# Kernel tuning notes

Measured on AMD Instinct MI355X. Metric: run time of the kernel, lower is better.

Reference implementation:

```python
import jax, jax.numpy as jnp
import numpy as np

B, NV, NQ, D, H = 8, 1024, 512, 1024, 8
HEAD_DIM = D // H


def _linear(x, W, b):
    # torch nn.Linear: x @ W.T + b, W: [out, in]
    return x @ W.T + b


def setup_inputs() -> dict:
    key = jax.random.key(0)
    ks = jax.random.split(key, 10)
    s = 0.02
    f32 = jnp.float32
    return {
        "v": jax.random.normal(ks[0], (B, NV, D), f32),
        "q": jax.random.normal(ks[1], (B, NQ, D), f32),
        "Wg_v4q": jax.random.normal(ks[2], (D, D), f32) * s,
        "bg_v4q": jnp.zeros((D,), f32),
        "Wg_q4v": jax.random.normal(ks[3], (D, D), f32) * s,
        "bg_q4v": jnp.zeros((D,), f32),
        "Wv": jax.random.normal(ks[4], (3 * D, D), f32) * s,
        "bv": jnp.zeros((3 * D,), f32),
        "Wq": jax.random.normal(ks[5], (3 * D, D), f32) * s,
        "bq": jnp.zeros((3 * D,), f32),
        "Wvo": jax.random.normal(ks[6], (D, D), f32) * s,
        "bvo": jnp.zeros((D,), f32),
        "Wqo": jax.random.normal(ks[7], (D, D), f32) * s,
        "bqo": jnp.zeros((D,), f32),
    }


def _mha(qh, kh, vh):
    # qh/kh/vh: [B, N, D] -> head-batched attention, faithful to per-head loop + concat
    b, n, _ = qh.shape
    m = kh.shape[1]
    qh = qh.reshape(b, n, H, HEAD_DIM)
    kh = kh.reshape(b, m, H, HEAD_DIM)
    vh = vh.reshape(b, m, H, HEAD_DIM)
    scores = jnp.einsum("bnhd,bmhd->bhnm", qh, kh) / jnp.sqrt(jnp.float32(HEAD_DIM))
    attn = jax.nn.softmax(scores, axis=-1)
    out = jnp.einsum("bhnm,bmhd->bnhd", attn, vh)
    return out.reshape(b, n, D)


def reference(v, q, Wg_v4q, bg_v4q, Wg_q4v, bg_q4v, Wv, bv, Wq, bq, Wvo, bvo, Wqo, bqo):
    # DyIntraModalityUpdate.forward (drop=0.0)
    v_mean = v.mean(axis=1)
    q_mean = q.mean(axis=1)
    v4q_gate = jax.nn.sigmoid(_linear(jax.nn.relu(v_mean), Wg_v4q, bg_v4q))[:, None, :]
    q4v_gate = jax.nn.sigmoid(_linear(jax.nn.relu(q_mean), Wg_q4v, bg_q4v))[:, None, :]
    v_trans = _linear(jax.nn.relu(v), Wv, bv)
    q_trans = _linear(jax.nn.relu(q), Wq, bq)
    v_k, v_q, v_v = jnp.split(v_trans, 3, axis=2)
    q_k, q_q, q_v = jnp.split(q_trans, 3, axis=2)
    new_vq = (1.0 + q4v_gate) * v_q
    new_vk = (1.0 + q4v_gate) * v_k
    new_qq = (1.0 + v4q_gate) * q_q
    new_qk = (1.0 + v4q_gate) * q_k
    v_update = _mha(new_vq, new_vk, v_v)
    q_update = _mha(new_qq, new_qk, q_v)
    updated_v = _linear(v + v_update, Wvo, bvo)
    updated_q = _linear(q + q_update, Wqo, bqo)
    return (updated_v, updated_q)
```

## Files before the change

kernel.cpp:

```cpp
#include <hip/hip_runtime.h>

typedef unsigned short u16;
typedef unsigned int u32;
typedef __attribute__((ext_vector_type(8))) short short8;
typedef __attribute__((ext_vector_type(4))) float floatx4;

__device__ __forceinline__ float bf2f(u16 x) {
    union { u32 u; float f; } c; c.u = ((u32)x) << 16; return c.f;
}
__device__ __forceinline__ u16 f2bf(float f) {
    union { float f; u32 u; } c; c.f = f;
    return (u16)((c.u + 0x7FFFu + ((c.u >> 16) & 1u)) >> 16);
}
__device__ __forceinline__ u32 pack_bf16(float lo, float hi) {
    return ((u32)f2bf(lo)) | (((u32)f2bf(hi)) << 16);
}

#define GLD_LDS(g, l) __builtin_amdgcn_global_load_lds( \
    (const __attribute__((address_space(1))) u32*)(g),  \
    (__attribute__((address_space(3))) u32*)(l), 16, 0, 0)


__global__ void cvt_kernel(const float* __restrict__ src, u16* __restrict__ dst,
                           int n8, int do_relu) {
    int i = blockIdx.x * 256 + threadIdx.x;
    if (i >= n8) return;
    float4 a = ((const float4*)src)[2 * i];
    float4 b = ((const float4*)src)[2 * i + 1];
    float v[8] = {a.x, a.y, a.z, a.w, b.x, b.y, b.z, b.w};
    short8 o;
#pragma unroll
    for (int j = 0; j < 8; j++) {
        float x = v[j];
        if (do_relu) x = fmaxf(x, 0.f);
        o[j] = (short)f2bf(x);
    }
    ((short8*)dst)[i] = o;
}


__global__ void mean_kernel(const float* __restrict__ x, float* __restrict__ out,
                            int N, int chunk) {
    int idx = blockIdx.x * 256 + threadIdx.x;
    int b = idx >> 10, d = idx & 1023;
    int nlo = blockIdx.y * chunk;
    const float* p = x + (size_t)b * N * 1024 + (size_t)nlo * 1024 + d;
    float s = 0.f;
    for (int n = 0; n < chunk; n++) s += p[(size_t)n * 1024];
    atomicAdd(out + idx, s * (1.0f / (float)N));
}

__global__ __launch_bounds__(256) void gate_kernel(const float* __restrict__ mean,
                                                   const float* __restrict__ Wg,
                                                   const float* __restrict__ bg,
                                                   float* __restrict__ gout) {
    int gw = blockIdx.x * 4 + (threadIdx.x >> 6);
    int lane = threadIdx.x & 63;
    int b = gw >> 10, n = gw & 1023;
    const float* wr = Wg + (size_t)n * 1024;
    const float* mr = mean + b * 1024;
    float acc = 0.f;
    for (int k = lane; k < 1024; k += 64)
        acc += fmaxf(mr[k], 0.f) * wr[k];
#pragma unroll
    for (int m = 1; m < 64; m <<= 1) acc += __shfl_xor(acc, m, 64);
    if (lane == 0) {
        float xg = acc + bg[n];
        gout[gw] = 1.f + 1.f / (1.f + __expf(-xg));
    }
}


__global__ __launch_bounds__(256) void gemm_bt_kernel(
    const u16* __restrict__ A, const u16* __restrict__ W,
    const float* __restrict__ bias, const float* __restrict__ gate,
    u16* __restrict__ Ch, float* __restrict__ Cf,
    int M, int N, int K, int seq, int gateN)
{
    __shared__ u16 As[2][128 * 32];
    __shared__ u16 Bs[2][128 * 32];

    const int tid = threadIdx.x;
    const int wave = tid >> 6, lane = tid & 63, quad = lane >> 4, l15 = lane & 15;

    const u32 gx = gridDim.x;
    const u32 flat = blockIdx.y * gx + blockIdx.x;
    const u32 per = (gx * gridDim.y) >> 3;
    const u32 swz = (flat & 7) * per + (flat >> 3);
    const int m0 = (int)(swz / gx) * 128, n0 = (int)(swz % gx) * 128;

    const int wm = (wave >> 1) * 64, wn = (wave & 1) * 64;

    floatx4 acc[4][4] = {};

    const int e0 = (wave * 1024 + lane * 16) >> 1;
    const int sr0 = e0 >> 5, sc0 = e0 & 31;
    const int e1 = e0 + 2048;
    const int sr1 = e1 >> 5, sc1 = e1 & 31;
    const size_t aoff0 = (size_t)(m0 + sr0) * K + sc0;
    const size_t aoff1 = (size_t)(m0 + sr1) * K + sc1;
    const size_t boff0 = (size_t)(n0 + sr0) * K + sc0;
    const size_t boff1 = (size_t)(n0 + sr1) * K + sc1;

    GLD_LDS(A + aoff0, As[0] + wave * 512);
    GLD_LDS(A + aoff1, As[0] + 2048 + wave * 512);
    GLD_LDS(W + boff0, Bs[0] + wave * 512);
    GLD_LDS(W + boff1, Bs[0] + 2048 + wave * 512);
    __syncthreads();

    int cur = 0;
    for (int k0 = 0; k0 < K; k0 += 32) {
        const int nxt = cur ^ 1;
        if (k0 + 32 < K) {
            GLD_LDS(A + aoff0 + k0 + 32, As[nxt] + wave * 512);
            GLD_LDS(A + aoff1 + k0 + 32, As[nxt] + 2048 + wave * 512);
            GLD_LDS(W + boff0 + k0 + 32, Bs[nxt] + wave * 512);
            GLD_LDS(W + boff1 + k0 + 32, Bs[nxt] + 2048 + wave * 512);
        }

        short8 af[4], bfr[4];
#pragma unroll
        for (int i = 0; i < 4; i++) {
            af[i]  = *(const short8*)(As[cur] + (wm + i * 16 + l15) * 32 + quad * 8);
            bfr[i] = *(const short8*)(Bs[cur] + (wn + i * 16 + l15) * 32 + quad * 8);
        }
#pragma unroll
        for (int mi = 0; mi < 4; mi++)
#pragma unroll
            for (int ni = 0; ni < 4; ni++)
                acc[mi][ni] = __builtin_amdgcn_mfma_f32_16x16x32_bf16(af[mi], bfr[ni], acc[mi][ni], 0, 0, 0);
        __syncthreads();
        cur = nxt;
    }

    const int b = m0 / seq;
#pragma unroll
    for (int ni = 0; ni < 4; ni++) {
        const int ncol = n0 + wn + ni * 16 + l15;
        const float bsv = bias[ncol];
        float g = 1.f;
        if (gate != nullptr && ncol < gateN) g = gate[b * 1024 + (ncol & 1023)];
#pragma unroll
        for (int mi = 0; mi < 4; mi++) {
            const int row = m0 + wm + mi * 16 + quad * 4;
#pragma unroll
            for (int r = 0; r < 4; r++) {
                float val = (acc[mi][ni][r] + bsv) * g;
                size_t idx = (size_t)(row + r) * N + ncol;
                if (Cf) Cf[idx] = val; else Ch[idx] = f2bf(val);
            }
        }
    }
}


__global__ __launch_bounds__(512, 2) void attn_kernel(
    const u16* __restrict__ T, const float* __restrict__ X,
    u16* __restrict__ U, int N)
{
    __shared__ __align__(16) u16 Ks[2][64 * 128];
    __shared__ __align__(16) u16 Vs[2][128 * 64];

    const int tid = threadIdx.x;
    const int wave = tid >> 6, lane = tid & 63, quad = (lane >> 4) & 3, l15 = lane & 15;

    const int f = blockIdx.y * gridDim.x + blockIdx.x;
    const int i3 = f >> 3;
    const int qb = i3 % gridDim.x;
    const int bh = (f & 7) * 8 + i3 / gridDim.x;
    const int b = bh >> 3, h = bh & 7;

    const size_t base = (size_t)b * N * 3072;
    const int kcol = h * 128, qcol = 1024 + h * 128, vcol = 2048 + h * 128;

    short8 qf[4];
    const int qrow0 = qb * 128 + wave * 16;
#pragma unroll
    for (int c = 0; c < 4; c++)
        qf[c] = *(const short8*)(T + base + (size_t)(qrow0 + l15) * 3072
                                   + qcol + c * 32 + quad * 8);

    floatx4 o[8] = {};
    float mrow = -1e30f, lrow = 0.f;
    const float scale = 0.08838834764831845f;

    int kst_kv[2], kst_d[2];
#pragma unroll
    for (int r = 0; r < 2; r++) {
        int ob = r * 8192 + wave * 1024 + lane * 16;
        int kv = ob >> 8;
        kst_kv[r] = kv;
        kst_d[r] = ((((ob >> 4) & 15) ^ (kv & 15)) << 3);
    }
    const int vkv = (tid & 31) * 2;
    const int vd8 = tid >> 5;

    short8 v0, v1;
#pragma unroll
    for (int r = 0; r < 2; r++)
        GLD_LDS(T + base + (size_t)kst_kv[r] * 3072 + kcol + kst_d[r],
                Ks[0] + r * 4096 + wave * 512);
    {
        const u16* vp = T + base + (size_t)vkv * 3072 + vcol + vd8 * 8;
        v0 = *(const short8*)vp;
        v1 = *(const short8*)(vp + 3072);
    }
#pragma unroll
    for (int j = 0; j < 8; j++) {
        u32 wv = ((u32)(u16)v0[j]) | (((u32)(u16)v1[j]) << 16);
        *(u32*)((char*)Vs[0] + (size_t)(vd8 * 8 + j) * 128
                + ((((vkv >> 3) ^ j)) << 4) + ((vkv * 2) & 15)) = wv;
    }
    __syncthreads();

    int cur = 0;
    for (int kt = 0; kt < N; kt += 64) {
        const int nxt = cur ^ 1;
        const bool more = (kt + 64) < N;

        if (more) {
#pragma unroll
            for (int r = 0; r < 2; r++)
                GLD_LDS(T + base + (size_t)(kt + 64 + kst_kv[r]) * 3072 + kcol + kst_d[r],
                        Ks[nxt] + r * 4096 + wave * 512);
            const u16* vp = T + base + (size_t)(kt + 64 + vkv) * 3072 + vcol + vd8 * 8;
            v0 = *(const short8*)vp;
            v1 = *(const short8*)(vp + 3072);
        }

        float p[4][4];
        __builtin_amdgcn_s_setprio(1);
#pragma unroll
        for (int ni = 0; ni < 4; ni++) {
            short8 kf[4];
#pragma unroll
            for (int c = 0; c < 4; c++)
                kf[c] = *(const short8*)(Ks[cur] + (ni * 16 + l15) * 128
                                            + (((c * 4 + quad) ^ l15) << 3));
            floatx4 s = {0.f, 0.f, 0.f, 0.f};
#pragma unroll
            for (int c = 0; c < 4; c++)
                s = __builtin_amdgcn_mfma_f32_16x16x32_bf16(kf[c], qf[c], s, 0, 0, 0);
#pragma unroll
            for (int r = 0; r < 4; r++) p[ni][r] = s[r] * scale;
        }
        __builtin_amdgcn_s_setprio(0);

        {
            float tm = p[0][0];
#pragma unroll
            for (int ni = 0; ni < 4; ni++)
#pragma unroll
                for (int r = 0; r < 4; r++) tm = fmaxf(tm, p[ni][r]);
            tm = fmaxf(tm, __shfl_xor(tm, 16, 64));
            tm = fmaxf(tm, __shfl_xor(tm, 32, 64));
            const bool need = __any(tm > mrow + 8.f);
            if (need) {
                float mnew = fmaxf(mrow, tm);
                float alpha = __expf(mrow - mnew);
                mrow = mnew;
                float ps = 0.f;
#pragma unroll
                for (int ni = 0; ni < 4; ni++)
#pragma unroll
                    for (int r = 0; r < 4; r++) {
                        float pe = __expf(p[ni][r] - mnew);
                        p[ni][r] = pe;
                        ps += pe;
                    }
                ps += __shfl_xor(ps, 16, 64);
                ps += __shfl_xor(ps, 32, 64);
                lrow = lrow * alpha + ps;
#pragma unroll
                for (int r = 0; r < 4; r++) {
                    float ab = __shfl(alpha, quad * 4 + r, 64);
#pragma unroll
                    for (int nt = 0; nt < 8; nt++) o[nt][r] *= ab;
                }
            } else {
                float ps = 0.f;
#pragma unroll
                for (int ni = 0; ni < 4; ni++)
#pragma unroll
                    for (int r = 0; r < 4; r++) {
                        float pe = __expf(p[ni][r] - mrow);
                        p[ni][r] = pe;
                        ps += pe;
                    }
                ps += __shfl_xor(ps, 16, 64);
                ps += __shfl_xor(ps, 32, 64);
                lrow += ps;
            }
        }

        u32* pw = (u32*)((char*)Vs[nxt] + wave * 2048);
        const int xs = (l15 & 7) << 2;
#pragma unroll
        for (int ni = 0; ni < 4; ni++)
#pragma unroll
            for (int s2 = 0; s2 < 2; s2++)
                pw[l15 * 32 + ((ni * 8 + quad * 2 + s2) ^ xs)]
                    = pack_bf16(p[ni][2 * s2], p[ni][2 * s2 + 1]);
        short8 pf[2];
#pragma unroll
        for (int kc = 0; kc < 2; kc++)
            pf[kc] = *(const short8*)(pw + l15 * 32 + ((kc * 16 + quad * 4) ^ xs));

        __builtin_amdgcn_s_setprio(1);
#pragma unroll
        for (int nt = 0; nt < 8; nt++) {
#pragma unroll
            for (int kc = 0; kc < 2; kc++) {
                short8 vf = *(const short8*)(Vs[cur] + (nt * 16 + l15) * 64
                                + (((kc * 4 + quad) ^ (l15 & 7)) << 3));
                o[nt] = __builtin_amdgcn_mfma_f32_16x16x32_bf16(pf[kc], vf, o[nt], 0, 0, 0);
            }
        }
        __builtin_amdgcn_s_setprio(0);

        if (more) {
#pragma unroll
            for (int j = 0; j < 8; j++) {
                u32 wv = ((u32)(u16)v0[j]) | (((u32)(u16)v1[j]) << 16);
                *(u32*)((char*)Vs[nxt] + (size_t)(vd8 * 8 + j) * 128
                        + ((((vkv >> 3) ^ j)) << 4) + ((vkv * 2) & 15)) = wv;
            }
        }
        __syncthreads();
        cur = nxt;
    }

    const size_t ub = (size_t)b * N * 1024;
#pragma unroll
    for (int r = 0; r < 4; r++) {
        float lb = __shfl(lrow, quad * 4 + r, 64);
        float inv = 1.f / lb;
        const size_t row = qb * 128 + wave * 16 + quad * 4 + r;
#pragma unroll
        for (int nt = 0; nt < 8; nt++) {
            const size_t idx = ub + row * 1024 + h * 128 + nt * 16 + l15;
            U[idx] = f2bf(X[idx] + o[nt][r] * inv);
        }
    }
}


extern "C" void kernel_launch(void* const* d_in, const int* in_sizes, int n_in,
                              void* d_out, int out_size, void* d_ws, size_t ws_size,
                              hipStream_t stream) {
    (void)in_sizes; (void)n_in; (void)out_size; (void)ws_size;
    const float* v   = (const float*)d_in[0];
    const float* q   = (const float*)d_in[1];
    const float* Wg_v4q = (const float*)d_in[2];
    const float* bg_v4q = (const float*)d_in[3];
    const float* Wg_q4v = (const float*)d_in[4];
    const float* bg_q4v = (const float*)d_in[5];
    const float* Wv  = (const float*)d_in[6];
    const float* bv  = (const float*)d_in[7];
    const float* Wq  = (const float*)d_in[8];
    const float* bq  = (const float*)d_in[9];
    const float* Wvo = (const float*)d_in[10];
    const float* bvo = (const float*)d_in[11];
    const float* Wqo = (const float*)d_in[12];
    const float* bqo = (const float*)d_in[13];
    float* out = (float*)d_out;

    char* w = (char*)d_ws;
    float* vmean = (float*)(w + 0);
    float* qmean = (float*)(w + 32768);
    float* gv4q  = (float*)(w + 65536);
    float* gq4v  = (float*)(w + 98304);
    u16* cWt  = (u16*)(w + (1 << 20));
    u16* cWo  = (u16*)(w + (1 << 20) + 6291456);
    u16* aReg = (u16*)(w + (16 << 20));
    u16* tReg = (u16*)(w + (32 << 20));

    hipMemsetAsync(vmean, 0, 65536, stream);
    mean_kernel<<<dim3(32, 8), 256, 0, stream>>>(v, vmean, 1024, 128);
    mean_kernel<<<dim3(32, 8), 256, 0, stream>>>(q, qmean, 512, 64);
    gate_kernel<<<2048, 256, 0, stream>>>(vmean, Wg_v4q, bg_v4q, gv4q);
    gate_kernel<<<2048, 256, 0, stream>>>(qmean, Wg_q4v, bg_q4v, gq4v);

    u16* crq  = aReg;
    u16* qt   = tReg;
    u16* qres = aReg;
    cvt_kernel<<<2048, 256, 0, stream>>>(q, crq, 524288, 1);
    cvt_kernel<<<1536, 256, 0, stream>>>(Wq, cWt, 393216, 0);
    cvt_kernel<<<512, 256, 0, stream>>>(Wqo, cWo, 131072, 0);
    gemm_bt_kernel<<<dim3(24, 32), 256, 0, stream>>>(crq, cWt, bq, gv4q, qt, nullptr,
                                                     4096, 3072, 1024, 512, 2048);
    attn_kernel<<<dim3(4, 64), 512, 0, stream>>>(qt, q, qres, 512);
    gemm_bt_kernel<<<dim3(8, 32), 256, 0, stream>>>(qres, cWo, bqo, nullptr, nullptr,
                                                    out + 8388608, 4096, 1024, 1024, 512, 0);

    u16* crv  = aReg;
    u16* vt   = tReg;
    u16* vres = aReg;
    cvt_kernel<<<4096, 256, 0, stream>>>(v, crv, 1048576, 1);
    cvt_kernel<<<1536, 256, 0, stream>>>(Wv, cWt, 393216, 0);
    cvt_kernel<<<512, 256, 0, stream>>>(Wvo, cWo, 131072, 0);
    gemm_bt_kernel<<<dim3(24, 64), 256, 0, stream>>>(crv, cWt, bv, gq4v, vt, nullptr,
                                                     8192, 3072, 1024, 1024, 2048);
    attn_kernel<<<dim3(8, 64), 512, 0, stream>>>(vt, v, vres, 1024);
    gemm_bt_kernel<<<dim3(8, 64), 256, 0, stream>>>(vres, cWo, bvo, nullptr, nullptr,
                                                    out, 8192, 1024, 1024, 1024, 0);
}
```

Measured before the change: 538.4 us.

## Fuse mean reduction with relu-bf16 conversion and batch gate and weight-convert launches

Mean computation for v and q now happens in the same pass that converts the activations to relu'd bf16. Partial sums go to a per-chunk buffer instead of atomics, which also removes the memset. The two gate GEMVs are merged into one launch, and the paired weight conversions are merged as well. This cuts a full extra read of v and q plus several launches. The cost is column-strided 2-byte stores in the fused kernel and a larger workspace so both converted activation buffers can exist at once.

```diff
diff --git a/kernel.cpp b/kernel.cpp
--- a/kernel.cpp
+++ b/kernel.cpp
@@ -21,53 +21,79 @@
     (__attribute__((address_space(3))) u32*)(l), 16, 0, 0)
 
 
-__global__ void cvt_kernel(const float* __restrict__ src, u16* __restrict__ dst,
-                           int n8, int do_relu) {
-    int i = blockIdx.x * 256 + threadIdx.x;
-    if (i >= n8) return;
-    float4 a = ((const float4*)src)[2 * i];
-    float4 b = ((const float4*)src)[2 * i + 1];
-    float v[8] = {a.x, a.y, a.z, a.w, b.x, b.y, b.z, b.w};
-    short8 o;
-#pragma unroll
-    for (int j = 0; j < 8; j++) {
-        float x = v[j];
-        if (do_relu) x = fmaxf(x, 0.f);
-        o[j] = (short)f2bf(x);
-    }
-    ((short8*)dst)[i] = o;
-}
-
-
-__global__ void mean_kernel(const float* __restrict__ x, float* __restrict__ out,
-                            int N, int chunk) {
-    int idx = blockIdx.x * 256 + threadIdx.x;
-    int b = idx >> 10, d = idx & 1023;
-    int nlo = blockIdx.y * chunk;
-    const float* p = x + (size_t)b * N * 1024 + (size_t)nlo * 1024 + d;
+__global__ __launch_bounds__(256) void meancvt_kernel(
+    const float* __restrict__ v, const float* __restrict__ q,
+    u16* __restrict__ crv, u16* __restrict__ crq, float* __restrict__ pmean)
+{
+    const int idx = blockIdx.x * 256 + threadIdx.x;
+    const int j = blockIdx.y;
+    const int half = idx >> 13;
+    const int lidx = idx & 8191;
+    const int b = lidx >> 10, d = lidx & 1023;
     float s = 0.f;
-    for (int n = 0; n < chunk; n++) s += p[(size_t)n * 1024];
-    atomicAdd(out + idx, s * (1.0f / (float)N));
-}
-
-__global__ __launch_bounds__(256) void gate_kernel(const float* __restrict__ mean,
-                                                   const float* __restrict__ Wg,
-                                                   const float* __restrict__ bg,
-                                                   float* __restrict__ gout) {
+    if (half == 0) {
+        const float* p = v + (size_t)b * 1024 * 1024 + (size_t)(j * 128) * 1024 + d;
+        u16* cw = crv + (size_t)b * 1024 * 1024 + (size_t)(j * 128) * 1024 + d;
+        for (int n = 0; n < 128; n++) {
+            float x = p[(size_t)n * 1024];
+            cw[(size_t)n * 1024] = f2bf(fmaxf(x, 0.f));
+            s += x;
+        }
+    } else {
+        const float* p = q + (size_t)b * 512 * 1024 + (size_t)(j * 64) * 1024 + d;
+        u16* cw = crq + (size_t)b * 512 * 1024 + (size_t)(j * 64) * 1024 + d;
+        for (int n = 0; n < 64; n++) {
+            float x = p[(size_t)n * 1024];
+            cw[(size_t)n * 1024] = f2bf(fmaxf(x, 0.f));
+            s += x;
+        }
+    }
+    pmean[j * 16384 + idx] = s;
+}
+
+
+__global__ __launch_bounds__(256) void gate_kernel(
+    const float* __restrict__ pmean,
+    const float* __restrict__ Wg0, const float* __restrict__ bg0, float* __restrict__ g0,
+    const float* __restrict__ Wg1, const float* __restrict__ bg1, float* __restrict__ g1)
+{
     int gw = blockIdx.x * 4 + (threadIdx.x >> 6);
     int lane = threadIdx.x & 63;
-    int b = gw >> 10, n = gw & 1023;
-    const float* wr = Wg + (size_t)n * 1024;
-    const float* mr = mean + b * 1024;
+    const int half = gw >> 13;
+    const int lw = gw & 8191;
+    const int b = lw >> 10, n = lw & 1023;
+    const float* wr = (half ? Wg1 : Wg0) + (size_t)n * 1024;
+    const float invN = half ? (1.f / 512.f) : (1.f / 1024.f);
+    const int pbase = half * 8192 + b * 1024;
     float acc = 0.f;
-    for (int k = lane; k < 1024; k += 64)
-        acc += fmaxf(mr[k], 0.f) * wr[k];
-#pragma unroll
-    for (int m = 1; m < 64; m <<= 1) acc += __shfl_xor(acc, m, 64);
+    for (int k = lane; k < 1024; k += 64) {
+        float m = 0.f;
+#pragma unroll
+        for (int j = 0; j < 8; j++) m += pmean[j * 16384 + pbase + k];
+        acc += fmaxf(m * invN, 0.f) * wr[k];
+    }
+#pragma unroll
+    for (int msk = 1; msk < 64; msk <<= 1) acc += __shfl_xor(acc, msk, 64);
     if (lane == 0) {
-        float xg = acc + bg[n];
-        gout[gw] = 1.f + 1.f / (1.f + __expf(-xg));
-    }
+        float xg = acc + (half ? bg1 : bg0)[n];
+        (half ? g1 : g0)[lw] = 1.f + 1.f / (1.f + __expf(-xg));
+    }
+}
+
+
+__global__ void wcvt_kernel(const float* __restrict__ Wt, const float* __restrict__ Wo,
+                            u16* __restrict__ cWt, u16* __restrict__ cWo) {
+    int i = blockIdx.x * 256 + threadIdx.x;
+    const float* src; u16* dst; int ii;
+    if (i < 393216) { src = Wt; dst = cWt; ii = i; }
+    else            { src = Wo; dst = cWo; ii = i - 393216; }
+    float4 a = ((const float4*)src)[2 * ii];
+    float4 b = ((const float4*)src)[2 * ii + 1];
+    float vv[8] = {a.x, a.y, a.z, a.w, b.x, b.y, b.z, b.w};
+    short8 o;
+#pragma unroll
+    for (int j = 0; j < 8; j++) o[j] = (short)f2bf(vv[j]);
+    ((short8*)dst)[ii] = o;
 }
 
 
@@ -366,39 +392,32 @@
     float* out = (float*)d_out;
 
     char* w = (char*)d_ws;
-    float* vmean = (float*)(w + 0);
-    float* qmean = (float*)(w + 32768);
-    float* gv4q  = (float*)(w + 65536);
-    float* gq4v  = (float*)(w + 98304);
-    u16* cWt  = (u16*)(w + (1 << 20));
-    u16* cWo  = (u16*)(w + (1 << 20) + 6291456);
-    u16* aReg = (u16*)(w + (16 << 20));
-    u16* tReg = (u16*)(w + (32 << 20));
-
-    hipMemsetAsync(vmean, 0, 65536, stream);
-    mean_kernel<<<dim3(32, 8), 256, 0, stream>>>(v, vmean, 1024, 128);
-    mean_kernel<<<dim3(32, 8), 256, 0, stream>>>(q, qmean, 512, 64);
-    gate_kernel<<<2048, 256, 0, stream>>>(vmean, Wg_v4q, bg_v4q, gv4q);
-    gate_kernel<<<2048, 256, 0, stream>>>(qmean, Wg_q4v, bg_q4v, gq4v);
-
-    u16* crq  = aReg;
+    float* pmean = (float*)(w + 0);
+    float* gv4q  = (float*)(w + 524288);
+    float* gq4v  = (float*)(w + 557056);
+    u16* cWt  = (u16*)(w + 1048576);
+    u16* cWo  = (u16*)(w + 7340032);
+    u16* tReg = (u16*)(w + 9437184);
+    u16* crq  = (u16*)(w + 34603008);
+    u16* crv  = (u16*)(w + 59768832);
+
     u16* qt   = tReg;
-    u16* qres = aReg;
-    cvt_kernel<<<2048, 256, 0, stream>>>(q, crq, 524288, 1);
-    cvt_kernel<<<1536, 256, 0, stream>>>(Wq, cWt, 393216, 0);
-    cvt_kernel<<<512, 256, 0, stream>>>(Wqo, cWo, 131072, 0);
+    u16* vt   = tReg;
+    u16* qres = crq;
+    u16* vres = crv;
+
+    meancvt_kernel<<<dim3(64, 8), 256, 0, stream>>>(v, q, crv, crq, pmean);
+    gate_kernel<<<4096, 256, 0, stream>>>(pmean, Wg_v4q, bg_v4q, gv4q,
+                                          Wg_q4v, bg_q4v, gq4v);
+
+    wcvt_kernel<<<2048, 256, 0, stream>>>(Wq, Wqo, cWt, cWo);
     gemm_bt_kernel<<<dim3(24, 32), 256, 0, stream>>>(crq, cWt, bq, gv4q, qt, nullptr,
                                                      4096, 3072, 1024, 512, 2048);
     attn_kernel<<<dim3(4, 64), 512, 0, stream>>>(qt, q, qres, 512);
     gemm_bt_kernel<<<dim3(8, 32), 256, 0, stream>>>(qres, cWo, bqo, nullptr, nullptr,
                                                     out + 8388608, 4096, 1024, 1024, 512, 0);
 
-    u16* crv  = aReg;
-    u16* vt   = tReg;
-    u16* vres = aReg;
-    cvt_kernel<<<4096, 256, 0, stream>>>(v, crv, 1048576, 1);
-    cvt_kernel<<<1536, 256, 0, stream>>>(Wv, cWt, 393216, 0);
-    cvt_kernel<<<512, 256, 0, stream>>>(Wvo, cWo, 131072, 0);
+    wcvt_kernel<<<2048, 256, 0, stream>>>(Wv, Wvo, cWt, cWo);
     gemm_bt_kernel<<<dim3(24, 64), 256, 0, stream>>>(crv, cWt, bv, gq4v, vt, nullptr,
                                                      8192, 3072, 1024, 1024, 2048);
     attn_kernel<<<dim3(8, 64), 512, 0, stream>>>(vt, v, vres, 1024);
```

New measurement: 459.2 us. 14.7% less time.
